# Optimization experiments

Measured on AMD Instinct MI355X. Metric: run time of the kernel, lower is better.

Reference implementation:

```python
import jax, jax.numpy as jnp
import numpy as np

NUM_EXPERTS = 8
SHARED = 1
TOP_K = 2
LB_WEIGHT = 0.01
Z_WEIGHT = 0.01


def setup_inputs() -> dict:
    key = jax.random.key(0)
    ks = jax.random.split(key, 8)
    B, S, H, I = 2, 1024, 1024, 4096
    E, SE = NUM_EXPERTS, SHARED
    sc = 0.02
    return {
        "hidden_states": jax.random.normal(ks[0], (B, S, H), jnp.float32),
        "router_w": jax.random.normal(ks[1], (E + SE, H), jnp.float32) * sc,
        "gate_w": jax.random.normal(ks[2], (E, I, H), jnp.float32) * sc,
        "up_w": jax.random.normal(ks[3], (E, I, H), jnp.float32) * sc,
        "down_w": jax.random.normal(ks[4], (E, H, I), jnp.float32) * sc,
        "shared_gate_w": jax.random.normal(ks[5], (SE, I, H), jnp.float32) * sc,
        "shared_up_w": jax.random.normal(ks[6], (SE, I, H), jnp.float32) * sc,
        "shared_down_w": jax.random.normal(ks[7], (SE, H, I), jnp.float32) * sc,
    }


def _swiglu(x, gw, uw, dw):
    # x: [T,H]; gw,uw: [I,H]; dw: [H,I]
    return (jax.nn.silu(x @ gw.T) * (x @ uw.T)) @ dw.T


def reference(hidden_states, router_w, gate_w, up_w, down_w,
              shared_gate_w, shared_up_w, shared_down_w):
    B, S, H = hidden_states.shape
    # Router over num_experts + shared_experts logits
    logits = jnp.einsum('bsh,eh->bse', hidden_states, router_w)  # [B,S,E+SE]
    probs = jax.nn.softmax(logits, axis=-1)
    w, sel = jax.lax.top_k(probs, TOP_K)                        # [B,S,K]
    w = w / (jnp.sum(w, axis=-1, keepdims=True) + 1e-6)

    xf = hidden_states.reshape(-1, H)    # [T,H]
    wf = w.reshape(-1, TOP_K)            # [T,K]
    sf = sel.reshape(-1, TOP_K)          # [T,K] int
    T = xf.shape[0]

    out = jnp.zeros_like(xf)
    loads = []
    for e in range(NUM_EXPERTS):
        m = (sf == e)                                     # [T,K]; top_k indices distinct
        we = jnp.sum(wf * m, axis=-1)                     # per-token weight for expert e
        y = _swiglu(xf, gate_w[e], up_w[e], down_w[e])    # dense; zero-weight tokens drop out
        out = out + we[:, None] * y
        loads.append(jnp.sum(jnp.any(m, axis=-1)).astype(jnp.float32))
    for s in range(SHARED):
        y = _swiglu(xf, shared_gate_w[s], shared_up_w[s], shared_down_w[s])
        out = out + y / SHARED
        loads.append(jnp.asarray(T, jnp.float32))
    loads = jnp.stack(loads)

    final = out.reshape(B, S, H)
    ln = loads / (jnp.sum(loads) + 1e-6)
    ideal = 1.0 / (NUM_EXPERTS + SHARED)
    load_balance_loss = jnp.mean((ln - ideal) ** 2)
    router_z_loss = jnp.mean(jnp.sum(logits ** 2, axis=-1))
    total_aux_loss = LB_WEIGHT * load_balance_loss + Z_WEIGHT * router_z_loss
    return final, total_aux_loss, load_balance_loss, router_z_loss
```

## Files before the change

kernel.cpp:

```cpp
#include <hip/hip_runtime.h>
#include <hip/hip_bf16.h>
#include <stdint.h>

#define T_TOK 2048
#define H_DIM 1024
#define I_DIM 4096

typedef __attribute__((ext_vector_type(8))) short bf16x8;
typedef __attribute__((ext_vector_type(4))) float f32x4;
typedef unsigned short u16;

__device__ __forceinline__ void gload_lds16(const void* g, void* l) {
  __builtin_amdgcn_global_load_lds((const __attribute__((address_space(1))) void*)g,
                                   (__attribute__((address_space(3))) void*)l, 16, 0, 0);
}

__device__ __forceinline__ u16 f2bf(float f) {
  uint32_t u = __float_as_uint(f);
  u += 0x7fff + ((u >> 16) & 1);
  return (u16)(u >> 16);
}

__device__ __forceinline__ bf16x8 lds_read_swz(const u16* base, int row, int kof) {
  int byt = (row * 64 + kof) * 2;
  byt ^= (row & 7) << 4;
  return *(const bf16x8*)((const char*)base + byt);
}

__global__ __launch_bounds__(256) void cvt_kernel(const float* __restrict__ s,
                                                  u16* __restrict__ d, int n) {
  int i = (blockIdx.x * 256 + threadIdx.x) * 8;
  int step = gridDim.x * 256 * 8;
  for (; i < n; i += step) {
    float4 v0 = *(const float4*)(s + i);
    float4 v1 = *(const float4*)(s + i + 4);
    union { u16 h[8]; uint4 q; } o;
    o.h[0] = f2bf(v0.x); o.h[1] = f2bf(v0.y); o.h[2] = f2bf(v0.z); o.h[3] = f2bf(v0.w);
    o.h[4] = f2bf(v1.x); o.h[5] = f2bf(v1.y); o.h[6] = f2bf(v1.z); o.h[7] = f2bf(v1.w);
    *(uint4*)(d + i) = o.q;
  }
}

__global__ __launch_bounds__(256) void router_kernel(
    const float* __restrict__ x, const float* __restrict__ rw,
    int* __restrict__ counts, int* __restrict__ lists, float* __restrict__ wlist,
    float* __restrict__ z_sum)
{
  int t = blockIdx.x;
  __shared__ float xs[H_DIM];
  __shared__ float red[9][4];
  const float* xp = x + (size_t)t * H_DIM;
  for (int h = threadIdx.x; h < H_DIM; h += 256) xs[h] = xp[h];
  __syncthreads();
  int lane = threadIdx.x & 63, wid = threadIdx.x >> 6;
  for (int e = 0; e < 9; ++e) {
    float p = 0.f;
    const float* rp = rw + e * H_DIM;
    for (int h = threadIdx.x; h < H_DIM; h += 256) p += xs[h] * rp[h];
#pragma unroll
    for (int off = 32; off > 0; off >>= 1) p += __shfl_down(p, off);
    if (lane == 0) red[e][wid] = p;
  }
  __syncthreads();
  if (threadIdx.x == 0) {
    float lg[9], m = -1e30f;
    for (int e = 0; e < 9; ++e) {
      lg[e] = red[e][0] + red[e][1] + red[e][2] + red[e][3];
      m = fmaxf(m, lg[e]);
    }
    float z = 0.f;
    for (int e = 0; e < 9; ++e) z += lg[e] * lg[e];
    atomicAdd(z_sum, z);
    float p[9], s = 0.f;
    for (int e = 0; e < 9; ++e) { p[e] = expf(lg[e] - m); s += p[e]; }
    int i0 = 0;
    for (int e = 1; e < 9; ++e) if (lg[e] > lg[i0]) i0 = e;
    int i1 = (i0 == 0) ? 1 : 0;
    for (int e = 0; e < 9; ++e) if (e != i0 && lg[e] > lg[i1]) i1 = e;
    float w0 = p[i0] / s, w1 = p[i1] / s;
    float inv = 1.f / (w0 + w1 + 1e-6f);
    w0 *= inv; w1 *= inv;
    if (i0 < 8) { int pos = atomicAdd(&counts[i0], 1); lists[i0 * T_TOK + pos] = t;            wlist[i0 * T_TOK + pos] = w0; }
    if (i1 < 8) { int pos = atomicAdd(&counts[i1], 1); lists[i1 * T_TOK + pos] = t | (1 << 12); wlist[i1 * T_TOK + pos] = w1; }
  }
}

__global__ void losses_kernel(const int* __restrict__ counts,
                              const float* __restrict__ z_sum,
                              float* __restrict__ outs) {
  if (threadIdx.x != 0 || blockIdx.x != 0) return;
  float loads[9]; float s = 0.f;
  for (int e = 0; e < 8; ++e) { loads[e] = (float)counts[e]; s += loads[e]; }
  loads[8] = (float)T_TOK; s += loads[8];
  float inv = 1.f / (s + 1e-6f);
  float ideal = 1.f / 9.f, lb = 0.f;
  for (int e = 0; e < 9; ++e) { float d = loads[e] * inv - ideal; lb += d * d; }
  lb /= 9.f;
  float zl = z_sum[0] / (float)T_TOK;
  outs[0] = 0.01f * lb + 0.01f * zl;
  outs[1] = lb;
  outs[2] = zl;
}

__global__ __launch_bounds__(256) void gateup_kernel(
    const u16* __restrict__ xb, const u16* __restrict__ gwb, const u16* __restrict__ upb,
    const int* __restrict__ lists, const int* __restrict__ counts, u16* __restrict__ hidden)
{
  int e = blockIdx.z;
  int count = (e == 8) ? T_TOK : counts[e];
  int m0 = blockIdx.y * 128;
  if (m0 >= count) return;
  int n0 = blockIdx.x * 64;
  const u16* gw = gwb + (size_t)e * I_DIM * H_DIM;
  const u16* uw = upb + (size_t)e * I_DIM * H_DIM;

  __shared__ __align__(16) u16 As[128 * 64];
  __shared__ __align__(16) u16 Bgs[64 * 64];
  __shared__ __align__(16) u16 Bus[64 * 64];
  __shared__ int tok_s[128];
  __shared__ int srow_s[128];

  int tid = threadIdx.x;
  if (tid < 128) {
    int rg = m0 + tid;
    int tok, srow;
    if (e == 8)            { tok = rg; srow = 2 * T_TOK + rg; }
    else if (rg < count)   { int p = lists[e * T_TOK + rg]; tok = p & 4095; srow = (p >> 12) * T_TOK + tok; }
    else                   { tok = 0; srow = 0; }
    tok_s[tid] = tok; srow_s[tid] = srow;
  }
  __syncthreads();

  const u16* asrc[4];
#pragma unroll
  for (int c = 0; c < 4; ++c) {
    int row = c * 32 + (tid >> 3);
    int col = ((tid & 7) ^ (row & 7)) * 8;
    asrc[c] = xb + (size_t)tok_s[row] * H_DIM + col;
  }
  const u16 *gsrc[2], *usrc[2];
#pragma unroll
  for (int c = 0; c < 2; ++c) {
    int row = c * 32 + (tid >> 3);
    int col = ((tid & 7) ^ (row & 7)) * 8;
    gsrc[c] = gw + (size_t)(n0 + row) * H_DIM + col;
    usrc[c] = uw + (size_t)(n0 + row) * H_DIM + col;
  }

  int lane = tid & 63, wid = tid >> 6;
  int wm = wid >> 1, wn = wid & 1;

  f32x4 accg[4][2] = {};
  f32x4 accu[4][2] = {};

  for (int kt = 0; kt < H_DIM / 64; ++kt) {
    int k0 = kt * 64;
#pragma unroll
    for (int c = 0; c < 4; ++c) gload_lds16(asrc[c] + k0, (void*)(As + c * 2048 + tid * 8));
#pragma unroll
    for (int c = 0; c < 2; ++c) {
      gload_lds16(gsrc[c] + k0, (void*)(Bgs + c * 2048 + tid * 8));
      gload_lds16(usrc[c] + k0, (void*)(Bus + c * 2048 + tid * 8));
    }
    __syncthreads();
#pragma unroll
    for (int kk = 0; kk < 2; ++kk) {
      bf16x8 a[4], bg[2], bu[2];
      int kof = kk * 32 + (lane >> 4) * 8;
#pragma unroll
      for (int mI = 0; mI < 4; ++mI)
        a[mI] = lds_read_swz(As, wm * 64 + mI * 16 + (lane & 15), kof);
#pragma unroll
      for (int nI = 0; nI < 2; ++nI) {
        bg[nI] = lds_read_swz(Bgs, wn * 32 + nI * 16 + (lane & 15), kof);
        bu[nI] = lds_read_swz(Bus, wn * 32 + nI * 16 + (lane & 15), kof);
      }
#pragma unroll
      for (int mI = 0; mI < 4; ++mI)
#pragma unroll
        for (int nI = 0; nI < 2; ++nI) {
          accg[mI][nI] = __builtin_amdgcn_mfma_f32_16x16x32_bf16(a[mI], bg[nI], accg[mI][nI], 0, 0, 0);
          accu[mI][nI] = __builtin_amdgcn_mfma_f32_16x16x32_bf16(a[mI], bu[nI], accu[mI][nI], 0, 0, 0);
        }
    }
    __syncthreads();
  }

#pragma unroll
  for (int mI = 0; mI < 4; ++mI) {
#pragma unroll
    for (int j = 0; j < 4; ++j) {
      int rloc = wm * 64 + mI * 16 + (lane >> 4) * 4 + j;
      int rg = m0 + rloc;
      if (rg >= count) continue;
      int srow = srow_s[rloc];
#pragma unroll
      for (int nI = 0; nI < 2; ++nI) {
        int i = n0 + wn * 32 + nI * 16 + (lane & 15);
        float g = accg[mI][nI][j], u = accu[mI][nI][j];
        float h = (g / (1.f + __expf(-g))) * u;
        hidden[(size_t)srow * I_DIM + i] = f2bf(h);
      }
    }
  }
}

__global__ __launch_bounds__(256) void down_kernel(
    const u16* __restrict__ hidden, const u16* __restrict__ dwb,
    const int* __restrict__ lists, const float* __restrict__ wlist,
    const int* __restrict__ counts, float* __restrict__ out)
{
  int e = blockIdx.z;
  int count = (e == 8) ? T_TOK : counts[e];
  int m0 = blockIdx.y * 64;
  if (m0 >= count) return;
  int n0 = blockIdx.x * 128;
  const u16* dw = dwb + (size_t)e * H_DIM * I_DIM;

  __shared__ __align__(16) u16 As[64 * 64];
  __shared__ __align__(16) u16 Bs[128 * 64];
  __shared__ int tok_s[64];
  __shared__ int srow_s[64];
  __shared__ float w_s[64];

  int tid = threadIdx.x;
  if (tid < 64) {
    int rg = m0 + tid;
    int tok, srow; float w;
    if (e == 8)          { tok = rg; srow = 2 * T_TOK + rg; w = 1.f; }
    else if (rg < count) { int p = lists[e * T_TOK + rg]; tok = p & 4095; srow = (p >> 12) * T_TOK + tok; w = wlist[e * T_TOK + rg]; }
    else                 { tok = 0; srow = 0; w = 0.f; }
    tok_s[tid] = tok; srow_s[tid] = srow; w_s[tid] = w;
  }
  __syncthreads();

  const u16* asrc[2];
#pragma unroll
  for (int c = 0; c < 2; ++c) {
    int row = c * 32 + (tid >> 3);
    int col = ((tid & 7) ^ (row & 7)) * 8;
    asrc[c] = hidden + (size_t)srow_s[row] * I_DIM + col;
  }
  const u16* bsrc[4];
#pragma unroll
  for (int c = 0; c < 4; ++c) {
    int row = c * 32 + (tid >> 3);
    int col = ((tid & 7) ^ (row & 7)) * 8;
    bsrc[c] = dw + (size_t)(n0 + row) * I_DIM + col;
  }

  int lane = tid & 63, wid = tid >> 6;
  int wm = wid >> 1, wn = wid & 1;

  f32x4 acc[2][4] = {};

  for (int kt = 0; kt < I_DIM / 64; ++kt) {
    int k0 = kt * 64;
#pragma unroll
    for (int c = 0; c < 2; ++c) gload_lds16(asrc[c] + k0, (void*)(As + c * 2048 + tid * 8));
#pragma unroll
    for (int c = 0; c < 4; ++c) gload_lds16(bsrc[c] + k0, (void*)(Bs + c * 2048 + tid * 8));
    __syncthreads();
#pragma unroll
    for (int kk = 0; kk < 2; ++kk) {
      bf16x8 a[2], b[4];
      int kof = kk * 32 + (lane >> 4) * 8;
#pragma unroll
      for (int mI = 0; mI < 2; ++mI)
        a[mI] = lds_read_swz(As, wm * 32 + mI * 16 + (lane & 15), kof);
#pragma unroll
      for (int nI = 0; nI < 4; ++nI)
        b[nI] = lds_read_swz(Bs, wn * 64 + nI * 16 + (lane & 15), kof);
#pragma unroll
      for (int mI = 0; mI < 2; ++mI)
#pragma unroll
        for (int nI = 0; nI < 4; ++nI)
          acc[mI][nI] = __builtin_amdgcn_mfma_f32_16x16x32_bf16(a[mI], b[nI], acc[mI][nI], 0, 0, 0);
    }
    __syncthreads();
  }

#pragma unroll
  for (int mI = 0; mI < 2; ++mI) {
#pragma unroll
    for (int j = 0; j < 4; ++j) {
      int rloc = wm * 32 + mI * 16 + (lane >> 4) * 4 + j;
      int rg = m0 + rloc;
      if (rg >= count) continue;
      int tok = tok_s[rloc];
      float w = w_s[rloc];
#pragma unroll
      for (int nI = 0; nI < 4; ++nI) {
        int h = n0 + wn * 64 + nI * 16 + (lane & 15);
        atomicAdd(&out[(size_t)tok * H_DIM + h], w * acc[mI][nI][j]);
      }
    }
  }
}

extern "C" void kernel_launch(void* const* d_in, const int* in_sizes, int n_in,
                              void* d_out, int out_size, void* d_ws, size_t ws_size,
                              hipStream_t stream)
{
  const float* x   = (const float*)d_in[0];
  const float* rw  = (const float*)d_in[1];
  const float* gw  = (const float*)d_in[2];
  const float* uw  = (const float*)d_in[3];
  const float* dw  = (const float*)d_in[4];
  const float* sgw = (const float*)d_in[5];
  const float* suw = (const float*)d_in[6];
  const float* sdw = (const float*)d_in[7];
  float* out = (float*)d_out;

  char* ws = (char*)d_ws;
  size_t off = 0;
  auto alloc = [&](size_t bytes) { void* p = ws + off; off += (bytes + 255) & ~255ULL; return p; };
  u16* xb     = (u16*)alloc((size_t)T_TOK * H_DIM * 2);
  u16* gwb    = (u16*)alloc((size_t)9 * I_DIM * H_DIM * 2);
  u16* upb    = (u16*)alloc((size_t)9 * I_DIM * H_DIM * 2);
  u16* dwb    = (u16*)alloc((size_t)9 * H_DIM * I_DIM * 2);
  u16* hidden = (u16*)alloc((size_t)3 * T_TOK * I_DIM * 2);
  int*   lists  = (int*)alloc(8 * T_TOK * 4);
  float* wl     = (float*)alloc(8 * T_TOK * 4);
  int*   counts = (int*)alloc(256);
  float* z_sum  = (float*)alloc(256);

  hipMemsetAsync(d_out, 0, (size_t)out_size * 4, stream);
  hipMemsetAsync(counts, 0, 512, stream);

  const int EW = I_DIM * H_DIM;
  cvt_kernel<<<2048, 256, 0, stream>>>(x,   xb, T_TOK * H_DIM);
  cvt_kernel<<<2048, 256, 0, stream>>>(gw,  gwb,            8 * EW);
  cvt_kernel<<<512,  256, 0, stream>>>(sgw, gwb + (size_t)8 * EW, EW);
  cvt_kernel<<<2048, 256, 0, stream>>>(uw,  upb,            8 * EW);
  cvt_kernel<<<512,  256, 0, stream>>>(suw, upb + (size_t)8 * EW, EW);
  cvt_kernel<<<2048, 256, 0, stream>>>(dw,  dwb,            8 * EW);
  cvt_kernel<<<512,  256, 0, stream>>>(sdw, dwb + (size_t)8 * EW, EW);

  router_kernel<<<T_TOK, 256, 0, stream>>>(x, rw, counts, lists, wl, z_sum);
  losses_kernel<<<1, 64, 0, stream>>>(counts, z_sum, out + (size_t)T_TOK * H_DIM);

  gateup_kernel<<<dim3(I_DIM / 64, T_TOK / 128, 9), 256, 0, stream>>>(xb, gwb, upb, lists, counts, hidden);
  down_kernel<<<dim3(H_DIM / 128, T_TOK / 64, 9), 256, 0, stream>>>(hidden, dwb, lists, wl, counts, out);
}
```

Measured before the change: 760.9 us.

## Convert expert weights to bf16 inside GEMM loads instead of separate passes

Removes the standalone fp32-to-bf16 conversion kernels for the gate, up and down expert weights. The GEMM kernels now read fp32 weights directly with vector loads, convert them in registers and store them swizzled into LDS. The down kernel tile is also reshaped to 128x64, matching the gate/up kernel. This avoids writing and re-reading roughly 300MB of converted weights per call, at the cost of doubling the bytes the GEMM tiles fetch for weights and giving up the async global-to-LDS path for them.

```diff
diff --git a/kernel.cpp b/kernel.cpp
--- a/kernel.cpp
+++ b/kernel.cpp
@@ -25,6 +25,17 @@
   int byt = (row * 64 + kof) * 2;
   byt ^= (row & 7) << 4;
   return *(const bf16x8*)((const char*)base + byt);
+}
+
+__device__ __forceinline__ void store16_swz(u16* base, int row, int colf,
+                                            float4 a, float4 b) {
+  union { __hip_bfloat162 h[4]; uint4 q; } o;
+  o.h[0] = __float22bfloat162_rn({a.x, a.y});
+  o.h[1] = __float22bfloat162_rn({a.z, a.w});
+  o.h[2] = __float22bfloat162_rn({b.x, b.y});
+  o.h[3] = __float22bfloat162_rn({b.z, b.w});
+  int byt = ((row * 64 + colf) * 2) ^ ((row & 7) << 4);
+  *(uint4*)((char*)base + byt) = o.q;
 }
 
 __global__ __launch_bounds__(256) void cvt_kernel(const float* __restrict__ s,
@@ -103,16 +114,20 @@
 }
 
 __global__ __launch_bounds__(256) void gateup_kernel(
-    const u16* __restrict__ xb, const u16* __restrict__ gwb, const u16* __restrict__ upb,
-    const int* __restrict__ lists, const int* __restrict__ counts, u16* __restrict__ hidden)
+    const u16* __restrict__ xb,
+    const float* __restrict__ gwf, const float* __restrict__ upf,
+    const float* __restrict__ sgwf, const float* __restrict__ suwf,
+    const int* __restrict__ lists, const int* __restrict__ counts,
+    u16* __restrict__ hidden)
 {
   int e = blockIdx.z;
   int count = (e == 8) ? T_TOK : counts[e];
   int m0 = blockIdx.y * 128;
   if (m0 >= count) return;
   int n0 = blockIdx.x * 64;
-  const u16* gw = gwb + (size_t)e * I_DIM * H_DIM;
-  const u16* uw = upb + (size_t)e * I_DIM * H_DIM;
+  const size_t EW = (size_t)I_DIM * H_DIM;
+  const float* gw = (e == 8) ? sgwf : gwf + (size_t)e * EW;
+  const float* uw = (e == 8) ? suwf : upf + (size_t)e * EW;
 
   __shared__ __align__(16) u16 As[128 * 64];
   __shared__ __align__(16) u16 Bgs[64 * 64];
@@ -138,13 +153,14 @@
     int col = ((tid & 7) ^ (row & 7)) * 8;
     asrc[c] = xb + (size_t)tok_s[row] * H_DIM + col;
   }
-  const u16 *gsrc[2], *usrc[2];
+  int brow[2], bcolf;
+  const float *gsrc[2], *usrc[2];
+  bcolf = (tid & 7) * 8;
 #pragma unroll
   for (int c = 0; c < 2; ++c) {
-    int row = c * 32 + (tid >> 3);
-    int col = ((tid & 7) ^ (row & 7)) * 8;
-    gsrc[c] = gw + (size_t)(n0 + row) * H_DIM + col;
-    usrc[c] = uw + (size_t)(n0 + row) * H_DIM + col;
+    brow[c] = c * 32 + (tid >> 3);
+    gsrc[c] = gw + (size_t)(n0 + brow[c]) * H_DIM + bcolf;
+    usrc[c] = uw + (size_t)(n0 + brow[c]) * H_DIM + bcolf;
   }
 
   int lane = tid & 63, wid = tid >> 6;
@@ -159,8 +175,12 @@
     for (int c = 0; c < 4; ++c) gload_lds16(asrc[c] + k0, (void*)(As + c * 2048 + tid * 8));
 #pragma unroll
     for (int c = 0; c < 2; ++c) {
-      gload_lds16(gsrc[c] + k0, (void*)(Bgs + c * 2048 + tid * 8));
-      gload_lds16(usrc[c] + k0, (void*)(Bus + c * 2048 + tid * 8));
+      float4 g0 = *(const float4*)(gsrc[c] + k0);
+      float4 g1 = *(const float4*)(gsrc[c] + k0 + 4);
+      float4 u0 = *(const float4*)(usrc[c] + k0);
+      float4 u1 = *(const float4*)(usrc[c] + k0 + 4);
+      store16_swz(Bgs, brow[c], bcolf, g0, g1);
+      store16_swz(Bus, brow[c], bcolf, u0, u1);
     }
     __syncthreads();
 #pragma unroll
@@ -206,25 +226,26 @@
 }
 
 __global__ __launch_bounds__(256) void down_kernel(
-    const u16* __restrict__ hidden, const u16* __restrict__ dwb,
+    const u16* __restrict__ hidden,
+    const float* __restrict__ dwf, const float* __restrict__ sdwf,
     const int* __restrict__ lists, const float* __restrict__ wlist,
     const int* __restrict__ counts, float* __restrict__ out)
 {
   int e = blockIdx.z;
   int count = (e == 8) ? T_TOK : counts[e];
-  int m0 = blockIdx.y * 64;
+  int m0 = blockIdx.y * 128;
   if (m0 >= count) return;
-  int n0 = blockIdx.x * 128;
-  const u16* dw = dwb + (size_t)e * H_DIM * I_DIM;
-
-  __shared__ __align__(16) u16 As[64 * 64];
-  __shared__ __align__(16) u16 Bs[128 * 64];
-  __shared__ int tok_s[64];
-  __shared__ int srow_s[64];
-  __shared__ float w_s[64];
+  int n0 = blockIdx.x * 64;
+  const float* dw = (e == 8) ? sdwf : dwf + (size_t)e * H_DIM * I_DIM;
+
+  __shared__ __align__(16) u16 As[128 * 64];
+  __shared__ __align__(16) u16 Bs[64 * 64];
+  __shared__ int tok_s[128];
+  __shared__ int srow_s[128];
+  __shared__ float w_s[128];
 
   int tid = threadIdx.x;
-  if (tid < 64) {
+  if (tid < 128) {
     int rg = m0 + tid;
     int tok, srow; float w;
     if (e == 8)          { tok = rg; srow = 2 * T_TOK + rg; w = 1.f; }
@@ -234,64 +255,68 @@
   }
   __syncthreads();
 
-  const u16* asrc[2];
-#pragma unroll
-  for (int c = 0; c < 2; ++c) {
+  const u16* asrc[4];
+#pragma unroll
+  for (int c = 0; c < 4; ++c) {
     int row = c * 32 + (tid >> 3);
     int col = ((tid & 7) ^ (row & 7)) * 8;
     asrc[c] = hidden + (size_t)srow_s[row] * I_DIM + col;
   }
-  const u16* bsrc[4];
-#pragma unroll
-  for (int c = 0; c < 4; ++c) {
-    int row = c * 32 + (tid >> 3);
-    int col = ((tid & 7) ^ (row & 7)) * 8;
-    bsrc[c] = dw + (size_t)(n0 + row) * I_DIM + col;
+  int brow[2], bcolf = (tid & 7) * 8;
+  const float* bsrc[2];
+#pragma unroll
+  for (int c = 0; c < 2; ++c) {
+    brow[c] = c * 32 + (tid >> 3);
+    bsrc[c] = dw + (size_t)(n0 + brow[c]) * I_DIM + bcolf;
   }
 
   int lane = tid & 63, wid = tid >> 6;
   int wm = wid >> 1, wn = wid & 1;
 
-  f32x4 acc[2][4] = {};
+  f32x4 acc[4][2] = {};
 
   for (int kt = 0; kt < I_DIM / 64; ++kt) {
     int k0 = kt * 64;
 #pragma unroll
-    for (int c = 0; c < 2; ++c) gload_lds16(asrc[c] + k0, (void*)(As + c * 2048 + tid * 8));
-#pragma unroll
-    for (int c = 0; c < 4; ++c) gload_lds16(bsrc[c] + k0, (void*)(Bs + c * 2048 + tid * 8));
+    for (int c = 0; c < 4; ++c) gload_lds16(asrc[c] + k0, (void*)(As + c * 2048 + tid * 8));
+#pragma unroll
+    for (int c = 0; c < 2; ++c) {
+      float4 b0 = *(const float4*)(bsrc[c] + k0);
+      float4 b1 = *(const float4*)(bsrc[c] + k0 + 4);
+      store16_swz(Bs, brow[c], bcolf, b0, b1);
+    }
     __syncthreads();
 #pragma unroll
     for (int kk = 0; kk < 2; ++kk) {
-      bf16x8 a[2], b[4];
+      bf16x8 a[4], b[2];
       int kof = kk * 32 + (lane >> 4) * 8;
 #pragma unroll
-      for (int mI = 0; mI < 2; ++mI)
-        a[mI] = lds_read_swz(As, wm * 32 + mI * 16 + (lane & 15), kof);
-#pragma unroll
-      for (int nI = 0; nI < 4; ++nI)
-        b[nI] = lds_read_swz(Bs, wn * 64 + nI * 16 + (lane & 15), kof);
-#pragma unroll
-      for (int mI = 0; mI < 2; ++mI)
-#pragma unroll
-        for (int nI = 0; nI < 4; ++nI)
+      for (int mI = 0; mI < 4; ++mI)
+        a[mI] = lds_read_swz(As, wm * 64 + mI * 16 + (lane & 15), kof);
+#pragma unroll
+      for (int nI = 0; nI < 2; ++nI)
+        b[nI] = lds_read_swz(Bs, wn * 32 + nI * 16 + (lane & 15), kof);
+#pragma unroll
+      for (int mI = 0; mI < 4; ++mI)
+#pragma unroll
+        for (int nI = 0; nI < 2; ++nI)
           acc[mI][nI] = __builtin_amdgcn_mfma_f32_16x16x32_bf16(a[mI], b[nI], acc[mI][nI], 0, 0, 0);
     }
     __syncthreads();
   }
 
 #pragma unroll
-  for (int mI = 0; mI < 2; ++mI) {
+  for (int mI = 0; mI < 4; ++mI) {
 #pragma unroll
     for (int j = 0; j < 4; ++j) {
-      int rloc = wm * 32 + mI * 16 + (lane >> 4) * 4 + j;
+      int rloc = wm * 64 + mI * 16 + (lane >> 4) * 4 + j;
       int rg = m0 + rloc;
       if (rg >= count) continue;
       int tok = tok_s[rloc];
       float w = w_s[rloc];
 #pragma unroll
-      for (int nI = 0; nI < 4; ++nI) {
-        int h = n0 + wn * 64 + nI * 16 + (lane & 15);
+      for (int nI = 0; nI < 2; ++nI) {
+        int h = n0 + wn * 32 + nI * 16 + (lane & 15);
         atomicAdd(&out[(size_t)tok * H_DIM + h], w * acc[mI][nI][j]);
       }
     }
@@ -316,9 +341,6 @@
   size_t off = 0;
   auto alloc = [&](size_t bytes) { void* p = ws + off; off += (bytes + 255) & ~255ULL; return p; };
   u16* xb     = (u16*)alloc((size_t)T_TOK * H_DIM * 2);
-  u16* gwb    = (u16*)alloc((size_t)9 * I_DIM * H_DIM * 2);
-  u16* upb    = (u16*)alloc((size_t)9 * I_DIM * H_DIM * 2);
-  u16* dwb    = (u16*)alloc((size_t)9 * H_DIM * I_DIM * 2);
   u16* hidden = (u16*)alloc((size_t)3 * T_TOK * I_DIM * 2);
   int*   lists  = (int*)alloc(8 * T_TOK * 4);
   float* wl     = (float*)alloc(8 * T_TOK * 4);
@@ -328,18 +350,12 @@
   hipMemsetAsync(d_out, 0, (size_t)out_size * 4, stream);
   hipMemsetAsync(counts, 0, 512, stream);
 
-  const int EW = I_DIM * H_DIM;
-  cvt_kernel<<<2048, 256, 0, stream>>>(x,   xb, T_TOK * H_DIM);
-  cvt_kernel<<<2048, 256, 0, stream>>>(gw,  gwb,            8 * EW);
-  cvt_kernel<<<512,  256, 0, stream>>>(sgw, gwb + (size_t)8 * EW, EW);
-  cvt_kernel<<<2048, 256, 0, stream>>>(uw,  upb,            8 * EW);
-  cvt_kernel<<<512,  256, 0, stream>>>(suw, upb + (size_t)8 * EW, EW);
-  cvt_kernel<<<2048, 256, 0, stream>>>(dw,  dwb,            8 * EW);
-  cvt_kernel<<<512,  256, 0, stream>>>(sdw, dwb + (size_t)8 * EW, EW);
-
+  cvt_kernel<<<1024, 256, 0, stream>>>(x, xb, T_TOK * H_DIM);
   router_kernel<<<T_TOK, 256, 0, stream>>>(x, rw, counts, lists, wl, z_sum);
   losses_kernel<<<1, 64, 0, stream>>>(counts, z_sum, out + (size_t)T_TOK * H_DIM);
 
-  gateup_kernel<<<dim3(I_DIM / 64, T_TOK / 128, 9), 256, 0, stream>>>(xb, gwb, upb, lists, counts, hidden);
-  down_kernel<<<dim3(H_DIM / 128, T_TOK / 64, 9), 256, 0, stream>>>(hidden, dwb, lists, wl, counts, out);
-}
+  gateup_kernel<<<dim3(I_DIM / 64, T_TOK / 128, 9), 256, 0, stream>>>(
+      xb, gw, uw, sgw, suw, lists, counts, hidden);
+  down_kernel<<<dim3(H_DIM / 64, T_TOK / 128, 9), 256, 0, stream>>>(
+      hidden, dw, sdw, lists, wl, counts, out);
+}
```

New measurement: 697.9 us. 1.09x faster.

## Double-buffer LDS in expert GEMMs, retile down kernel, fuse x conversion into router

Applied to the files above, without the earlier changes.

Both expert GEMM kernels now use two LDS buffers, so the next K tile is prefetched while the current one is being multiplied, leaving one barrier per step. The down projection tile changes from 64x128 to 128x64 to match the gate/up layout, and the bf16 conversion of the activations moves into the router kernel, removing one launch. These changes aim to hide global-load latency, at the cost of twice the LDS per block, which may lower occupancy.

```diff
diff --git a/kernel.cpp b/kernel.cpp
--- a/kernel.cpp
+++ b/kernel.cpp
@@ -44,7 +44,7 @@
 __global__ __launch_bounds__(256) void router_kernel(
     const float* __restrict__ x, const float* __restrict__ rw,
     int* __restrict__ counts, int* __restrict__ lists, float* __restrict__ wlist,
-    float* __restrict__ z_sum)
+    float* __restrict__ z_sum, u16* __restrict__ xb)
 {
   int t = blockIdx.x;
   __shared__ float xs[H_DIM];
@@ -52,6 +52,7 @@
   const float* xp = x + (size_t)t * H_DIM;
   for (int h = threadIdx.x; h < H_DIM; h += 256) xs[h] = xp[h];
   __syncthreads();
+  for (int h = threadIdx.x; h < H_DIM; h += 256) xb[(size_t)t * H_DIM + h] = f2bf(xs[h]);
   int lane = threadIdx.x & 63, wid = threadIdx.x >> 6;
   for (int e = 0; e < 9; ++e) {
     float p = 0.f;
@@ -114,9 +115,9 @@
   const u16* gw = gwb + (size_t)e * I_DIM * H_DIM;
   const u16* uw = upb + (size_t)e * I_DIM * H_DIM;
 
-  __shared__ __align__(16) u16 As[128 * 64];
-  __shared__ __align__(16) u16 Bgs[64 * 64];
-  __shared__ __align__(16) u16 Bus[64 * 64];
+  __shared__ __align__(16) u16 As[2][128 * 64];
+  __shared__ __align__(16) u16 Bgs[2][64 * 64];
+  __shared__ __align__(16) u16 Bus[2][64 * 64];
   __shared__ int tok_s[128];
   __shared__ int srow_s[128];
 
@@ -153,27 +154,43 @@
   f32x4 accg[4][2] = {};
   f32x4 accu[4][2] = {};
 
-  for (int kt = 0; kt < H_DIM / 64; ++kt) {
-    int k0 = kt * 64;
-#pragma unroll
-    for (int c = 0; c < 4; ++c) gload_lds16(asrc[c] + k0, (void*)(As + c * 2048 + tid * 8));
-#pragma unroll
-    for (int c = 0; c < 2; ++c) {
-      gload_lds16(gsrc[c] + k0, (void*)(Bgs + c * 2048 + tid * 8));
-      gload_lds16(usrc[c] + k0, (void*)(Bus + c * 2048 + tid * 8));
-    }
-    __syncthreads();
+  const int NK = H_DIM / 64;
+
+#pragma unroll
+  for (int c = 0; c < 4; ++c) gload_lds16(asrc[c], (void*)(As[0] + c * 2048 + tid * 8));
+#pragma unroll
+  for (int c = 0; c < 2; ++c) {
+    gload_lds16(gsrc[c], (void*)(Bgs[0] + c * 2048 + tid * 8));
+    gload_lds16(usrc[c], (void*)(Bus[0] + c * 2048 + tid * 8));
+  }
+  __syncthreads();
+
+  for (int kt = 0; kt < NK; ++kt) {
+    int cur = kt & 1, nxt = cur ^ 1;
+    if (kt + 1 < NK) {
+      int k1 = (kt + 1) * 64;
+#pragma unroll
+      for (int c = 0; c < 4; ++c) gload_lds16(asrc[c] + k1, (void*)(As[nxt] + c * 2048 + tid * 8));
+#pragma unroll
+      for (int c = 0; c < 2; ++c) {
+        gload_lds16(gsrc[c] + k1, (void*)(Bgs[nxt] + c * 2048 + tid * 8));
+        gload_lds16(usrc[c] + k1, (void*)(Bus[nxt] + c * 2048 + tid * 8));
+      }
+    }
+    const u16* cA = As[cur];
+    const u16* cBg = Bgs[cur];
+    const u16* cBu = Bus[cur];
 #pragma unroll
     for (int kk = 0; kk < 2; ++kk) {
       bf16x8 a[4], bg[2], bu[2];
       int kof = kk * 32 + (lane >> 4) * 8;
 #pragma unroll
       for (int mI = 0; mI < 4; ++mI)
-        a[mI] = lds_read_swz(As, wm * 64 + mI * 16 + (lane & 15), kof);
+        a[mI] = lds_read_swz(cA, wm * 64 + mI * 16 + (lane & 15), kof);
 #pragma unroll
       for (int nI = 0; nI < 2; ++nI) {
-        bg[nI] = lds_read_swz(Bgs, wn * 32 + nI * 16 + (lane & 15), kof);
-        bu[nI] = lds_read_swz(Bus, wn * 32 + nI * 16 + (lane & 15), kof);
+        bg[nI] = lds_read_swz(cBg, wn * 32 + nI * 16 + (lane & 15), kof);
+        bu[nI] = lds_read_swz(cBu, wn * 32 + nI * 16 + (lane & 15), kof);
       }
 #pragma unroll
       for (int mI = 0; mI < 4; ++mI)
@@ -212,19 +229,19 @@
 {
   int e = blockIdx.z;
   int count = (e == 8) ? T_TOK : counts[e];
-  int m0 = blockIdx.y * 64;
+  int m0 = blockIdx.y * 128;
   if (m0 >= count) return;
-  int n0 = blockIdx.x * 128;
+  int n0 = blockIdx.x * 64;
   const u16* dw = dwb + (size_t)e * H_DIM * I_DIM;
 
-  __shared__ __align__(16) u16 As[64 * 64];
-  __shared__ __align__(16) u16 Bs[128 * 64];
-  __shared__ int tok_s[64];
-  __shared__ int srow_s[64];
-  __shared__ float w_s[64];
+  __shared__ __align__(16) u16 As[2][128 * 64];
+  __shared__ __align__(16) u16 Bs[2][64 * 64];
+  __shared__ int tok_s[128];
+  __shared__ int srow_s[128];
+  __shared__ float w_s[128];
 
   int tid = threadIdx.x;
-  if (tid < 64) {
+  if (tid < 128) {
     int rg = m0 + tid;
     int tok, srow; float w;
     if (e == 8)          { tok = rg; srow = 2 * T_TOK + rg; w = 1.f; }
@@ -234,64 +251,76 @@
   }
   __syncthreads();
 
-  const u16* asrc[2];
+  const u16* asrc[4];
+#pragma unroll
+  for (int c = 0; c < 4; ++c) {
+    int row = c * 32 + (tid >> 3);
+    int col = ((tid & 7) ^ (row & 7)) * 8;
+    asrc[c] = hidden + (size_t)srow_s[row] * I_DIM + col;
+  }
+  const u16* bsrc[2];
 #pragma unroll
   for (int c = 0; c < 2; ++c) {
     int row = c * 32 + (tid >> 3);
     int col = ((tid & 7) ^ (row & 7)) * 8;
-    asrc[c] = hidden + (size_t)srow_s[row] * I_DIM + col;
-  }
-  const u16* bsrc[4];
-#pragma unroll
-  for (int c = 0; c < 4; ++c) {
-    int row = c * 32 + (tid >> 3);
-    int col = ((tid & 7) ^ (row & 7)) * 8;
     bsrc[c] = dw + (size_t)(n0 + row) * I_DIM + col;
   }
 
   int lane = tid & 63, wid = tid >> 6;
   int wm = wid >> 1, wn = wid & 1;
 
-  f32x4 acc[2][4] = {};
-
-  for (int kt = 0; kt < I_DIM / 64; ++kt) {
-    int k0 = kt * 64;
-#pragma unroll
-    for (int c = 0; c < 2; ++c) gload_lds16(asrc[c] + k0, (void*)(As + c * 2048 + tid * 8));
-#pragma unroll
-    for (int c = 0; c < 4; ++c) gload_lds16(bsrc[c] + k0, (void*)(Bs + c * 2048 + tid * 8));
+  f32x4 acc[4][2] = {};
+
+  const int NK = I_DIM / 64;
+
+#pragma unroll
+  for (int c = 0; c < 4; ++c) gload_lds16(asrc[c], (void*)(As[0] + c * 2048 + tid * 8));
+#pragma unroll
+  for (int c = 0; c < 2; ++c) gload_lds16(bsrc[c], (void*)(Bs[0] + c * 2048 + tid * 8));
+  __syncthreads();
+
+  for (int kt = 0; kt < NK; ++kt) {
+    int cur = kt & 1, nxt = cur ^ 1;
+    if (kt + 1 < NK) {
+      int k1 = (kt + 1) * 64;
+#pragma unroll
+      for (int c = 0; c < 4; ++c) gload_lds16(asrc[c] + k1, (void*)(As[nxt] + c * 2048 + tid * 8));
+#pragma unroll
+      for (int c = 0; c < 2; ++c) gload_lds16(bsrc[c] + k1, (void*)(Bs[nxt] + c * 2048 + tid * 8));
+    }
+    const u16* cA = As[cur];
+    const u16* cB = Bs[cur];
+#pragma unroll
+    for (int kk = 0; kk < 2; ++kk) {
+      bf16x8 a[4], b[2];
+      int kof = kk * 32 + (lane >> 4) * 8;
+#pragma unroll
+      for (int mI = 0; mI < 4; ++mI)
+        a[mI] = lds_read_swz(cA, wm * 64 + mI * 16 + (lane & 15), kof);
+#pragma unroll
+      for (int nI = 0; nI < 2; ++nI)
+        b[nI] = lds_read_swz(cB, wn * 32 + nI * 16 + (lane & 15), kof);
+#pragma unroll
+      for (int mI = 0; mI < 4; ++mI)
+#pragma unroll
+        for (int nI = 0; nI < 2; ++nI)
+          acc[mI][nI] = __builtin_amdgcn_mfma_f32_16x16x32_bf16(a[mI], b[nI], acc[mI][nI], 0, 0, 0);
+    }
     __syncthreads();
-#pragma unroll
-    for (int kk = 0; kk < 2; ++kk) {
-      bf16x8 a[2], b[4];
-      int kof = kk * 32 + (lane >> 4) * 8;
-#pragma unroll
-      for (int mI = 0; mI < 2; ++mI)
-        a[mI] = lds_read_swz(As, wm * 32 + mI * 16 + (lane & 15), kof);
-#pragma unroll
-      for (int nI = 0; nI < 4; ++nI)
-        b[nI] = lds_read_swz(Bs, wn * 64 + nI * 16 + (lane & 15), kof);
-#pragma unroll
-      for (int mI = 0; mI < 2; ++mI)
-#pragma unroll
-        for (int nI = 0; nI < 4; ++nI)
-          acc[mI][nI] = __builtin_amdgcn_mfma_f32_16x16x32_bf16(a[mI], b[nI], acc[mI][nI], 0, 0, 0);
-    }
-    __syncthreads();
-  }
-
-#pragma unroll
-  for (int mI = 0; mI < 2; ++mI) {
+  }
+
+#pragma unroll
+  for (int mI = 0; mI < 4; ++mI) {
 #pragma unroll
     for (int j = 0; j < 4; ++j) {
-      int rloc = wm * 32 + mI * 16 + (lane >> 4) * 4 + j;
+      int rloc = wm * 64 + mI * 16 + (lane >> 4) * 4 + j;
       int rg = m0 + rloc;
       if (rg >= count) continue;
       int tok = tok_s[rloc];
       float w = w_s[rloc];
 #pragma unroll
-      for (int nI = 0; nI < 4; ++nI) {
-        int h = n0 + wn * 64 + nI * 16 + (lane & 15);
+      for (int nI = 0; nI < 2; ++nI) {
+        int h = n0 + wn * 32 + nI * 16 + (lane & 15);
         atomicAdd(&out[(size_t)tok * H_DIM + h], w * acc[mI][nI][j]);
       }
     }
@@ -329,7 +358,6 @@
   hipMemsetAsync(counts, 0, 512, stream);
 
   const int EW = I_DIM * H_DIM;
-  cvt_kernel<<<2048, 256, 0, stream>>>(x,   xb, T_TOK * H_DIM);
   cvt_kernel<<<2048, 256, 0, stream>>>(gw,  gwb,            8 * EW);
   cvt_kernel<<<512,  256, 0, stream>>>(sgw, gwb + (size_t)8 * EW, EW);
   cvt_kernel<<<2048, 256, 0, stream>>>(uw,  upb,            8 * EW);
@@ -337,9 +365,11 @@
   cvt_kernel<<<2048, 256, 0, stream>>>(dw,  dwb,            8 * EW);
   cvt_kernel<<<512,  256, 0, stream>>>(sdw, dwb + (size_t)8 * EW, EW);
 
-  router_kernel<<<T_TOK, 256, 0, stream>>>(x, rw, counts, lists, wl, z_sum);
+  router_kernel<<<T_TOK, 256, 0, stream>>>(x, rw, counts, lists, wl, z_sum, xb);
   losses_kernel<<<1, 64, 0, stream>>>(counts, z_sum, out + (size_t)T_TOK * H_DIM);
 
-  gateup_kernel<<<dim3(I_DIM / 64, T_TOK / 128, 9), 256, 0, stream>>>(xb, gwb, upb, lists, counts, hidden);
-  down_kernel<<<dim3(H_DIM / 128, T_TOK / 64, 9), 256, 0, stream>>>(hidden, dwb, lists, wl, counts, out);
-}
+  gateup_kernel<<<dim3(I_DIM / 64, T_TOK / 128, 9), 256, 0, stream>>>(
+      xb, gwb, upb, lists, counts, hidden);
+  down_kernel<<<dim3(H_DIM / 64, T_TOK / 128, 9), 256, 0, stream>>>(
+      hidden, dwb, lists, wl, counts, out);
+}
```

Result: slower. 803.0 us (+5.5%).
